# Kernel tuning notes

Measured on AMD Instinct MI355X. Metric: run time of the kernel, lower is better.

Reference implementation:

```python
import jax, jax.numpy as jnp
import numpy as np

B, H, NQ, NK, DH, DD = 2, 16, 1024, 1024, 128, 8


def setup_inputs() -> dict:
    key = jax.random.key(0)
    ks = jax.random.split(key, 10)
    f = lambda kk, s: jax.random.normal(kk, s, dtype=jnp.float32)
    return {
        "q": f(ks[0], (B, H, NQ, DH)),
        "k": f(ks[1], (B, H, NK, DH)),
        "v": f(ks[2], (B, H, NK, DH)),
        "c": jnp.ones((1,), jnp.float32),  # leaky constant; unused (is_leaky=False)
        "d_q": f(ks[3], (B, NQ, DD)),
        "d_k_top": f(ks[4], (B, NK, DD)),
        "d_k_bot": f(ks[5], (B, NK, DD)),
        "d_k_score": jax.random.uniform(ks[6], (B, NK, 2, 1), dtype=jnp.float32),
        "w_w": f(ks[7], (DD, H)) * 0.1,
        "b_w": jnp.zeros((H,), jnp.float32),
        "w_b": f(ks[8], (DD, H)) * 0.1,
        "b_b": jnp.zeros((H,), jnp.float32),
    }


def reference(q, k, v, c, d_q, d_k_top, d_k_bot, d_k_score, w_w, b_w, w_b, b_b):
    # scaled dot-product scores: [B,H,Nq,Nk]
    scale = 1.0 / jnp.sqrt(jnp.asarray(q.shape[-1], q.dtype))
    scores = jnp.einsum('bhqd,bhkd->bhqk', q, k) * scale

    # pairwise relative maps: [B,Nq,Nk,2,Dd]
    dm = jnp.stack(
        [d_q[:, :, None, :] - d_k_top[:, None, :, :],
         d_q[:, :, None, :] - d_k_bot[:, None, :, :]], axis=3)
    # interpolate top/bot with sampler scores d_k_score [B,Nk,2,1] -> [B,Nq,Nk,Dd]
    dm = (dm * d_k_score[:, None]).sum(axis=3)

    # tiny per-head projections Dd -> H, then gate (softplus) and bias
    dw = jax.nn.softplus(dm @ w_w + b_w)        # [B,Nq,Nk,H]
    db = dm @ w_b + b_b                          # [B,Nq,Nk,H]
    scores = scores * dw.transpose(0, 3, 1, 2) + db.transpose(0, 3, 1, 2)

    p = jax.nn.softmax(scores, axis=-1)          # probability_function (non-leaky)
    out = p @ v                                  # [B,H,Nq,dh]
    return out, p
```

## Files before the change

kernel.cpp:

```cpp
#include <hip/hip_runtime.h>

typedef short short8 __attribute__((ext_vector_type(8)));
typedef float f32x4 __attribute__((ext_vector_type(4)));

constexpr int Bc = 2, Hc = 16, NQc = 1024, NKc = 1024, DHc = 128;
constexpr int BQ = 16;
constexpr int PBP = 1032;
constexpr size_t KBF_ELEMS = (size_t)Bc * Hc * NKc * DHc;

__device__ __forceinline__ unsigned cvtpk(float a, float b) {
  unsigned r;
  asm("v_cvt_pk_bf16_f32 %0, %1, %2" : "=v"(r) : "v"(a), "v"(b));
  return r;
}
__device__ __forceinline__ unsigned long long pack4(float a, float b, float c, float d) {
  return (unsigned long long)cvtpk(a, b) | ((unsigned long long)cvtpk(c, d) << 32);
}
__device__ __forceinline__ float bfbits(unsigned u) {
  union { unsigned x; float f; } w; w.x = u; return w.f;
}

typedef __attribute__((address_space(1))) const unsigned int glb_u32;
typedef __attribute__((address_space(3))) unsigned int lds_u32;
__device__ __forceinline__ void gl16(const void* g, void* l) {
  __builtin_amdgcn_global_load_lds((glb_u32*)g, (lds_u32*)l, 16, 0, 0);
}

__global__ __launch_bounds__(256) void prep(const float* __restrict__ km,
                                            const float* __restrict__ vm,
                                            unsigned short* __restrict__ kbf,
                                            unsigned short* __restrict__ vtb) {
  const int blk = blockIdx.x, t = threadIdx.x;
  if (blk < 1024) {
    __shared__ float tile[64][65];
    const int bh = blk >> 5, tl = blk & 31;
    const int k0 = (tl & 15) * 64, d0 = (tl >> 4) * 64;
    const float* vsrc = vm + ((size_t)bh * NKc + k0) * DHc + d0;
    {
      int j = t & 63, i0 = t >> 6;
#pragma unroll
      for (int s = 0; s < 16; ++s) {
        int i = i0 + s * 4;
        tile[i][j] = vsrc[(size_t)i * DHc + j];
      }
    }
    __syncthreads();
    unsigned short* vdst = vtb + ((size_t)bh * DHc + d0) * NKc + k0;
    {
      int i2 = (t & 15) * 4, j0 = t >> 4;
#pragma unroll
      for (int s = 0; s < 4; ++s) {
        int j2 = j0 + s * 16;
        float a0 = tile[i2 + 0][j2], a1 = tile[i2 + 1][j2];
        float a2 = tile[i2 + 2][j2], a3 = tile[i2 + 3][j2];
        *(unsigned long long*)(vdst + (size_t)j2 * NKc + i2) = pack4(a0, a1, a2, a3);
      }
    }
  } else {
    const float4* kf4 = (const float4*)km;
#pragma unroll
    for (int rep = 0; rep < 2; ++rep) {
      size_t g = (size_t)(blk - 1024) * 256 + t + (size_t)rep * 524288;
      float4 f = kf4[g];
      *(unsigned long long*)(kbf + g * 4) = pack4(f.x, f.y, f.z, f.w);
    }
  }
}

__global__ __launch_bounds__(512, 4) void attn_main(
    const float* __restrict__ qm, const unsigned short* __restrict__ kbf,
    const unsigned short* __restrict__ vtb,
    const float* __restrict__ dq, const float* __restrict__ dkt, const float* __restrict__ dkb,
    const float* __restrict__ dks, const float* __restrict__ ww, const float* __restrict__ bw,
    const float* __restrict__ wb, const float* __restrict__ bb,
    float* __restrict__ outp, float* __restrict__ pp)
{
  __shared__ __align__(16) unsigned short kv[16384];
  __shared__ __align__(16) unsigned short pbs[BQ * PBP];
  __shared__ float e0s[1024], cws[1024], cbs[1024];
  __shared__ float aws[BQ], abs_[BQ];
  __shared__ float redm[128], redl[128];

  const int wg = blockIdx.x;
  const int bid = (wg & 7) * 256 + (wg >> 3);
  const int qt = bid & 63, h = (bid >> 6) & 15, b = bid >> 10;
  const int q0 = qt * BQ;
  const int t = threadIdx.x, wv = t >> 6, lane = t & 63;
  const int hi = lane >> 4, lo = lane & 15;
  const int rb = hi << 2;
  const int bh = b * Hc + h;

  {
    float whc[8], wbc[8];
#pragma unroll
    for (int d = 0; d < 8; ++d) { whc[d] = ww[d * Hc + h]; wbc[d] = wb[d * Hc + h]; }
    float bwh = bw[h], bbh = bb[h];
#pragma unroll
    for (int rep = 0; rep < 2; ++rep) {
      int kk = t + rep * 512;
      const float* sc = dks + ((size_t)b * NKc + kk) * 2;
      float s0 = sc[0], s1 = sc[1];
      const float* tp = dkt + ((size_t)b * NKc + kk) * 8;
      const float* bp = dkb + ((size_t)b * NKc + kk) * 8;
      float4 t0 = *(const float4*)tp, t1 = *(const float4*)(tp + 4);
      float4 b0 = *(const float4*)bp, b1 = *(const float4*)(bp + 4);
      float tv[8] = {t0.x, t0.y, t0.z, t0.w, t1.x, t1.y, t1.z, t1.w};
      float bv[8] = {b0.x, b0.y, b0.z, b0.w, b1.x, b1.y, b1.z, b1.w};
      float cw = 0.f, cb = 0.f;
#pragma unroll
      for (int d = 0; d < 8; ++d) {
        float dk = tv[d] * s0 + bv[d] * s1;
        cw += dk * whc[d];
        cb += dk * wbc[d];
      }
      e0s[kk] = s0 + s1;
      cws[kk] = cw - bwh;
      cbs[kk] = cb - bbh;
    }
    if (t < BQ) {
      const float* dqr = dq + ((size_t)b * NQc + q0 + t) * 8;
      float4 a = *(const float4*)dqr, b4 = *(const float4*)(dqr + 4);
      float dv[8] = {a.x, a.y, a.z, a.w, b4.x, b4.y, b4.z, b4.w};
      float saw = 0.f, sab = 0.f;
#pragma unroll
      for (int d = 0; d < 8; ++d) { saw += dv[d] * whc[d]; sab += dv[d] * wbc[d]; }
      aws[t] = saw; abs_[t] = sab;
    }
  }

  short8 qf[4];
  {
    const float* qg = qm + ((size_t)bh * NQc + q0 + lo) * DHc + hi * 8;
#pragma unroll
    for (int kk = 0; kk < 4; ++kk) {
      float4 a = *(const float4*)(qg + kk * 32);
      float4 c = *(const float4*)(qg + kk * 32 + 4);
      union { short8 v; unsigned long long u[2]; } q8;
      q8.u[0] = pack4(a.x, a.y, a.z, a.w);
      q8.u[1] = pack4(c.x, c.y, c.z, c.w);
      qf[kk] = q8.v;
    }
  }

  const float scale = 0.08838834764831845f;
  const unsigned short* kg = kbf + (size_t)bh * NKc * DHc;
  const unsigned short* vtg = vtb + (size_t)bh * DHc * NKc;

  const unsigned short* ksrc[4];
  const unsigned short* vsrc[4];
  char* ldst[4];
#pragma unroll
  for (int r = 0; r < 4; ++r) {
    int base = ((r << 3) + wv) << 10;
    int F = base + (lane << 4);
    int kr = F >> 8;
    int gslot = ((F >> 4) & 15) ^ (kr & 15);
    ksrc[r] = kg + ((size_t)kr << 7) + (gslot << 3);
    vsrc[r] = vtg + ((size_t)kr << 10) + (gslot << 3);
    ldst[r] = (char*)kv + base;
  }
  const int kr16 = (wv << 4) + lo;
  int qoff[4];
#pragma unroll
  for (int kk = 0; kk < 4; ++kk)
    qoff[kk] = (kr16 << 7) + (((((kk << 2) + hi)) ^ (kr16 & 15)) << 3);

  __syncthreads();
  float aw4[4], ab4[4];
#pragma unroll
  for (int i = 0; i < 4; ++i) { aw4[i] = aws[rb + i]; ab4[i] = abs_[rb + i]; }

  f32x4 sacc[8];
#pragma unroll 1
  for (int kc = 0; kc < 8; ++kc) {
    __syncthreads();
#pragma unroll
    for (int r = 0; r < 4; ++r)
      gl16(ksrc[r] + ((size_t)kc << 14), ldst[r]);
    __syncthreads();
    f32x4 acc = {0.f, 0.f, 0.f, 0.f};
#pragma unroll
    for (int kk = 0; kk < 4; ++kk)
      acc = __builtin_amdgcn_mfma_f32_16x16x32_bf16(qf[kk], *(const short8*)&kv[qoff[kk]], acc, 0, 0, 0);
    int cg = (kc << 7) + kr16;
    float e0 = e0s[cg], cw2 = cws[cg], cb2 = cbs[cg];
#pragma unroll
    for (int i = 0; i < 4; ++i) {
      float s = acc[i] * scale;
      float x = fmaf(e0, aw4[i], -cw2);
      float ex = __expf(x);
      float sp = (x > 20.f) ? x : __logf(1.f + ex);
      acc[i] = fmaf(s, sp, fmaf(e0, ab4[i], -cb2));
    }
    sacc[kc] = acc;
  }

  float m4[4], inv4[4];
#pragma unroll
  for (int i = 0; i < 4; ++i) {
    float pm = sacc[0][i];
#pragma unroll
    for (int kc = 1; kc < 8; ++kc) pm = fmaxf(pm, sacc[kc][i]);
    pm = fmaxf(pm, __shfl_xor(pm, 1, 64));
    pm = fmaxf(pm, __shfl_xor(pm, 2, 64));
    pm = fmaxf(pm, __shfl_xor(pm, 4, 64));
    pm = fmaxf(pm, __shfl_xor(pm, 8, 64));
    m4[i] = pm;
  }
  if (lo == 0) {
#pragma unroll
    for (int i = 0; i < 4; ++i) redm[(wv << 4) + rb + i] = m4[i];
  }
  __syncthreads();
#pragma unroll
  for (int i = 0; i < 4; ++i) {
    float m = redm[rb + i];
#pragma unroll
    for (int w = 1; w < 8; ++w) m = fmaxf(m, redm[(w << 4) + rb + i]);
    m4[i] = m;
  }
#pragma unroll
  for (int i = 0; i < 4; ++i) {
    float pl = 0.f;
#pragma unroll
    for (int kc = 0; kc < 8; ++kc) {
      float e = __expf(sacc[kc][i] - m4[i]);
      sacc[kc][i] = e;
      pl += e;
    }
    pl += __shfl_xor(pl, 1, 64);
    pl += __shfl_xor(pl, 2, 64);
    pl += __shfl_xor(pl, 4, 64);
    pl += __shfl_xor(pl, 8, 64);
    inv4[i] = pl;
  }
  if (lo == 0) {
#pragma unroll
    for (int i = 0; i < 4; ++i) redl[(wv << 4) + rb + i] = inv4[i];
  }
  __syncthreads();
#pragma unroll
  for (int i = 0; i < 4; ++i) {
    float l = redl[rb + i];
#pragma unroll
    for (int w = 1; w < 8; ++w) l += redl[(w << 4) + rb + i];
    inv4[i] = 1.f / l;
  }
#pragma unroll
  for (int i = 0; i < 4; ++i) {
    int prow = (rb + i) * PBP + kr16;
    float iv = inv4[i];
#pragma unroll
    for (int k2 = 0; k2 < 4; ++k2) {
      unsigned u = cvtpk(sacc[2 * k2][i] * iv, sacc[2 * k2 + 1][i] * iv);
      pbs[prow + ((2 * k2) << 7)] = (unsigned short)u;
      pbs[prow + ((2 * k2 + 1) << 7)] = (unsigned short)(u >> 16);
    }
  }

  const int pA = lo * PBP + (hi << 3);
  const int prow_w = t >> 5, pc4 = (t & 31) * 4;
  const unsigned short* pbr = &pbs[prow_w * PBP + pc4];
  float* pgl = pp + ((size_t)bh * NQc + q0 + prow_w) * (size_t)NKc + pc4;
  f32x4 oacc = {0.f, 0.f, 0.f, 0.f};
#pragma unroll 1
  for (int vc = 0; vc < 8; ++vc) {
    __syncthreads();
#pragma unroll
    for (int r = 0; r < 4; ++r)
      gl16(vsrc[r] + (vc << 7), ldst[r]);
    {
      unsigned long long u = *(const unsigned long long*)(pbr + (vc << 7));
      unsigned l32 = (unsigned)u, h32 = (unsigned)(u >> 32);
      float4 o;
      o.x = bfbits(l32 << 16);
      o.y = bfbits(l32 & 0xffff0000u);
      o.z = bfbits(h32 << 16);
      o.w = bfbits(h32 & 0xffff0000u);
      *(float4*)(pgl + (vc << 7)) = o;
    }
    __syncthreads();
#pragma unroll
    for (int kt = 0; kt < 4; ++kt) {
      short8 af = *(const short8*)&pbs[pA + (vc << 7) + (kt << 5)];
      short8 bf = *(const short8*)&kv[qoff[kt]];
      oacc = __builtin_amdgcn_mfma_f32_16x16x32_bf16(af, bf, oacc, 0, 0, 0);
    }
  }

#pragma unroll
  for (int i = 0; i < 4; ++i)
    outp[((size_t)bh * NQc + q0 + rb + i) * DHc + kr16] = oacc[i];
}

extern "C" void kernel_launch(void* const* d_in, const int* in_sizes, int n_in,
                              void* d_out, int out_size, void* d_ws, size_t ws_size,
                              hipStream_t stream) {
  (void)in_sizes; (void)n_in; (void)out_size; (void)ws_size;
  const float* q   = (const float*)d_in[0];
  const float* k   = (const float*)d_in[1];
  const float* v   = (const float*)d_in[2];
  const float* dq  = (const float*)d_in[4];
  const float* dkt = (const float*)d_in[5];
  const float* dkb = (const float*)d_in[6];
  const float* dks = (const float*)d_in[7];
  const float* ww  = (const float*)d_in[8];
  const float* bw  = (const float*)d_in[9];
  const float* wb  = (const float*)d_in[10];
  const float* bb  = (const float*)d_in[11];
  float* outp = (float*)d_out;
  float* pp   = outp + (size_t)Bc * Hc * NQc * DHc;

  unsigned short* kbf = (unsigned short*)d_ws;
  unsigned short* vtb = kbf + KBF_ELEMS;

  hipLaunchKernelGGL(prep, dim3(3072), dim3(256), 0, stream, k, v, kbf, vtb);
  hipLaunchKernelGGL(attn_main, dim3(2048), dim3(512), 0, stream,
                     q, kbf, vtb, dq, dkt, dkb, dks, ww, bw, wb, bb, outp, pp);
}
```

Before: 278.3 us.

## Double-buffer K/V LDS tiles with manual vmcnt waits and raw barriers

Splits the K/V LDS staging area into two buffers and issues global-to-LDS loads two chunks ahead, so memory transfers overlap with MFMA and softplus work. The next V chunks are prefetched during the final score iterations. Full __syncthreads calls are replaced with explicit s_waitcnt vmcnt/lgkmcnt plus s_barrier so waits can be partial. The extra 32KB of LDS lowers the occupancy hint from 4 to 2 blocks per CU, and the hand-counted vmcnt values interact with the p global stores, which makes correctness fragile.

```diff
diff --git a/kernel.cpp b/kernel.cpp
--- a/kernel.cpp
+++ b/kernel.cpp
@@ -7,6 +7,11 @@
 constexpr int BQ = 16;
 constexpr int PBP = 1032;
 constexpr size_t KBF_ELEMS = (size_t)Bc * Hc * NKc * DHc;
+
+#define BARRIER() __builtin_amdgcn_s_barrier()
+#define WAITV(n) asm volatile("s_waitcnt vmcnt(" #n ")" ::: "memory")
+#define WAITL0() asm volatile("s_waitcnt lgkmcnt(0)" ::: "memory")
+#define SCHED0() __builtin_amdgcn_sched_barrier(0)
 
 __device__ __forceinline__ unsigned cvtpk(float a, float b) {
   unsigned r;
@@ -67,7 +72,7 @@
   }
 }
 
-__global__ __launch_bounds__(512, 4) void attn_main(
+__global__ __launch_bounds__(512, 2) void attn_main(
     const float* __restrict__ qm, const unsigned short* __restrict__ kbf,
     const unsigned short* __restrict__ vtb,
     const float* __restrict__ dq, const float* __restrict__ dkt, const float* __restrict__ dkb,
@@ -75,7 +80,7 @@
     const float* __restrict__ wb, const float* __restrict__ bb,
     float* __restrict__ outp, float* __restrict__ pp)
 {
-  __shared__ __align__(16) unsigned short kv[16384];
+  __shared__ __align__(16) unsigned short kv[2][16384];
   __shared__ __align__(16) unsigned short pbs[BQ * PBP];
   __shared__ float e0s[1024], cws[1024], cbs[1024];
   __shared__ float aws[BQ], abs_[BQ];
@@ -148,7 +153,7 @@
 
   const unsigned short* ksrc[4];
   const unsigned short* vsrc[4];
-  char* ldst[4];
+  int boff[4];
 #pragma unroll
   for (int r = 0; r < 4; ++r) {
     int base = ((r << 3) + wv) << 10;
@@ -157,7 +162,7 @@
     int gslot = ((F >> 4) & 15) ^ (kr & 15);
     ksrc[r] = kg + ((size_t)kr << 7) + (gslot << 3);
     vsrc[r] = vtg + ((size_t)kr << 10) + (gslot << 3);
-    ldst[r] = (char*)kv + base;
+    boff[r] = base;
   }
   const int kr16 = (wv << 4) + lo;
   int qoff[4];
@@ -169,19 +174,22 @@
   float aw4[4], ab4[4];
 #pragma unroll
   for (int i = 0; i < 4; ++i) { aw4[i] = aws[rb + i]; ab4[i] = abs_[rb + i]; }
+
+#pragma unroll
+  for (int r = 0; r < 4; ++r) gl16(ksrc[r], (char*)&kv[0][0] + boff[r]);
+#pragma unroll
+  for (int r = 0; r < 4; ++r) gl16(ksrc[r] + (1 << 14), (char*)&kv[1][0] + boff[r]);
 
   f32x4 sacc[8];
 #pragma unroll 1
   for (int kc = 0; kc < 8; ++kc) {
-    __syncthreads();
-#pragma unroll
-    for (int r = 0; r < 4; ++r)
-      gl16(ksrc[r] + ((size_t)kc << 14), ldst[r]);
-    __syncthreads();
+    const int cur = kc & 1;
+    WAITV(4); SCHED0();
+    BARRIER();
     f32x4 acc = {0.f, 0.f, 0.f, 0.f};
 #pragma unroll
     for (int kk = 0; kk < 4; ++kk)
-      acc = __builtin_amdgcn_mfma_f32_16x16x32_bf16(qf[kk], *(const short8*)&kv[qoff[kk]], acc, 0, 0, 0);
+      acc = __builtin_amdgcn_mfma_f32_16x16x32_bf16(qf[kk], *(const short8*)&kv[cur][qoff[kk]], acc, 0, 0, 0);
     int cg = (kc << 7) + kr16;
     float e0 = e0s[cg], cw2 = cws[cg], cb2 = cbs[cg];
 #pragma unroll
@@ -193,6 +201,16 @@
       acc[i] = fmaf(s, sp, fmaf(e0, ab4[i], -cb2));
     }
     sacc[kc] = acc;
+    WAITL0(); SCHED0();
+    BARRIER();
+    if (kc < 6) {
+#pragma unroll
+      for (int r = 0; r < 4; ++r) gl16(ksrc[r] + ((size_t)(kc + 2) << 14), (char*)&kv[cur][0] + boff[r]);
+    } else {
+      int vc0 = kc - 6;
+#pragma unroll
+      for (int r = 0; r < 4; ++r) gl16(vsrc[r] + (vc0 << 7), (char*)&kv[cur][0] + boff[r]);
+    }
   }
 
   float m4[4], inv4[4];
@@ -211,7 +229,7 @@
 #pragma unroll
     for (int i = 0; i < 4; ++i) redm[(wv << 4) + rb + i] = m4[i];
   }
-  __syncthreads();
+  WAITL0(); SCHED0(); BARRIER();
 #pragma unroll
   for (int i = 0; i < 4; ++i) {
     float m = redm[rb + i];
@@ -238,7 +256,7 @@
 #pragma unroll
     for (int i = 0; i < 4; ++i) redl[(wv << 4) + rb + i] = inv4[i];
   }
-  __syncthreads();
+  WAITL0(); SCHED0(); BARRIER();
 #pragma unroll
   for (int i = 0; i < 4; ++i) {
     float l = redl[rb + i];
@@ -257,6 +275,7 @@
       pbs[prow + ((2 * k2 + 1) << 7)] = (unsigned short)(u >> 16);
     }
   }
+  WAITL0();
 
   const int pA = lo * PBP + (hi << 3);
   const int prow_w = t >> 5, pc4 = (t & 31) * 4;
@@ -264,27 +283,35 @@
   float* pgl = pp + ((size_t)bh * NQc + q0 + prow_w) * (size_t)NKc + pc4;
   f32x4 oacc = {0.f, 0.f, 0.f, 0.f};
 #pragma unroll 1
-  for (int vc = 0; vc < 8; ++vc) {
-    __syncthreads();
-#pragma unroll
-    for (int r = 0; r < 4; ++r)
-      gl16(vsrc[r] + (vc << 7), ldst[r]);
+  for (int vc = 8; vc < 16; ++vc) {
+    const int cur = vc & 1;
+    const int vc0 = vc - 8;
+    if (vc == 8)      { WAITV(4); }
+    else if (vc == 15){ WAITV(1); }
+    else              { WAITV(5); }
+    SCHED0();
+    BARRIER();
+#pragma unroll
+    for (int kt = 0; kt < 4; ++kt) {
+      short8 af = *(const short8*)&pbs[pA + (vc0 << 7) + (kt << 5)];
+      short8 bf = *(const short8*)&kv[cur][qoff[kt]];
+      oacc = __builtin_amdgcn_mfma_f32_16x16x32_bf16(af, bf, oacc, 0, 0, 0);
+    }
     {
-      unsigned long long u = *(const unsigned long long*)(pbr + (vc << 7));
+      unsigned long long u = *(const unsigned long long*)(pbr + (vc0 << 7));
       unsigned l32 = (unsigned)u, h32 = (unsigned)(u >> 32);
       float4 o;
       o.x = bfbits(l32 << 16);
       o.y = bfbits(l32 & 0xffff0000u);
       o.z = bfbits(h32 << 16);
       o.w = bfbits(h32 & 0xffff0000u);
-      *(float4*)(pgl + (vc << 7)) = o;
-    }
-    __syncthreads();
-#pragma unroll
-    for (int kt = 0; kt < 4; ++kt) {
-      short8 af = *(const short8*)&pbs[pA + (vc << 7) + (kt << 5)];
-      short8 bf = *(const short8*)&kv[qoff[kt]];
-      oacc = __builtin_amdgcn_mfma_f32_16x16x32_bf16(af, bf, oacc, 0, 0, 0);
+      *(float4*)(pgl + (vc0 << 7)) = o;
+    }
+    WAITL0(); SCHED0();
+    BARRIER();
+    if (vc0 + 2 < 8) {
+#pragma unroll
+      for (int r = 0; r < 4; ++r) gl16(vsrc[r] + ((vc0 + 2) << 7), (char*)&kv[cur][0] + boff[r]);
     }
   }
 
```

Result: slower. 319.2 us (+14.7%).

## Pre-swizzle K/V into MFMA fragment order and load directly to registers

Applied to the files above, without the earlier changes.

The prep kernel now writes bf16 K and V in the exact per-lane MFMA fragment order, so attn_main loads operands straight from global memory into registers with double-buffered prefetch instead of staging them through LDS with global_load_lds. The large P buffer in LDS is replaced by a small double-buffered per-chunk tile, and the P store to global is software-pipelined one chunk behind. Barriers become raw s_barrier calls with explicit lgkmcnt waits. This removes LDS staging and most block-wide syncs and shrinks LDS use, which may raise occupancy, but it increases register pressure and relies on uncoalesced-looking fragment loads being cached well.

```diff
diff --git a/kernel.cpp b/kernel.cpp
--- a/kernel.cpp
+++ b/kernel.cpp
@@ -5,8 +5,12 @@
 
 constexpr int Bc = 2, Hc = 16, NQc = 1024, NKc = 1024, DHc = 128;
 constexpr int BQ = 16;
-constexpr int PBP = 1032;
-constexpr size_t KBF_ELEMS = (size_t)Bc * Hc * NKc * DHc;
+constexpr int PBP = 136;
+constexpr size_t FRAG_ELEMS = (size_t)Bc * Hc * NKc * DHc;
+
+#define BARRIER() __builtin_amdgcn_s_barrier()
+#define WAITL0() asm volatile("s_waitcnt lgkmcnt(0)" ::: "memory")
+#define SCHED0() __builtin_amdgcn_sched_barrier(0)
 
 __device__ __forceinline__ unsigned cvtpk(float a, float b) {
   unsigned r;
@@ -20,16 +24,10 @@
   union { unsigned x; float f; } w; w.x = u; return w.f;
 }
 
-typedef __attribute__((address_space(1))) const unsigned int glb_u32;
-typedef __attribute__((address_space(3))) unsigned int lds_u32;
-__device__ __forceinline__ void gl16(const void* g, void* l) {
-  __builtin_amdgcn_global_load_lds((glb_u32*)g, (lds_u32*)l, 16, 0, 0);
-}
-
 __global__ __launch_bounds__(256) void prep(const float* __restrict__ km,
                                             const float* __restrict__ vm,
-                                            unsigned short* __restrict__ kbf,
-                                            unsigned short* __restrict__ vtb) {
+                                            unsigned short* __restrict__ kf2,
+                                            unsigned short* __restrict__ vf2) {
   const int blk = blockIdx.x, t = threadIdx.x;
   if (blk < 1024) {
     __shared__ float tile[64][65];
@@ -45,38 +43,48 @@
       }
     }
     __syncthreads();
-    unsigned short* vdst = vtb + ((size_t)bh * DHc + d0) * NKc + k0;
-    {
-      int i2 = (t & 15) * 4, j0 = t >> 4;
-#pragma unroll
-      for (int s = 0; s < 4; ++s) {
-        int j2 = j0 + s * 16;
-        float a0 = tile[i2 + 0][j2], a1 = tile[i2 + 1][j2];
-        float a2 = tile[i2 + 2][j2], a3 = tile[i2 + 3][j2];
-        *(unsigned long long*)(vdst + (size_t)j2 * NKc + i2) = pack4(a0, a1, a2, a3);
-      }
+    const int vc = k0 >> 7, ktb = (k0 >> 5) & 3, wvb = d0 >> 4;
+    unsigned short* vdst = vf2 + ((size_t)bh << 17);
+#pragma unroll
+    for (int s2 = 0; s2 < 2; ++s2) {
+      int ts = s2 * 256 + t;
+      int wvl = ts >> 7, ktl = (ts >> 6) & 1, hii = (ts >> 4) & 3, loo = ts & 15;
+      int seg = ((vc * 4 + ktb + ktl) * 8 + wvb + wvl) * 64 + (hii << 4) + loo;
+      int kl = ktl * 32 + hii * 8;
+      int dl = wvl * 16 + loo;
+      float a0 = tile[kl + 0][dl], a1 = tile[kl + 1][dl], a2 = tile[kl + 2][dl], a3 = tile[kl + 3][dl];
+      float a4 = tile[kl + 4][dl], a5 = tile[kl + 5][dl], a6 = tile[kl + 6][dl], a7 = tile[kl + 7][dl];
+      unsigned long long u0 = pack4(a0, a1, a2, a3), u1 = pack4(a4, a5, a6, a7);
+      *(unsigned long long*)(vdst + (size_t)seg * 8) = u0;
+      *(unsigned long long*)(vdst + (size_t)seg * 8 + 4) = u1;
     }
   } else {
-    const float4* kf4 = (const float4*)km;
-#pragma unroll
-    for (int rep = 0; rep < 2; ++rep) {
-      size_t g = (size_t)(blk - 1024) * 256 + t + (size_t)rep * 524288;
-      float4 f = kf4[g];
-      *(unsigned long long*)(kbf + g * 4) = pack4(f.x, f.y, f.z, f.w);
+    const int blk2 = blk - 1024;
+    const int bh = blk2 >> 3, kc = blk2 & 7;
+    const float* ks = km + ((size_t)bh * NKc + kc * 128) * DHc;
+    unsigned short* kdst = kf2 + ((size_t)(bh * 8 + kc)) * 16384;
+#pragma unroll
+    for (int s8 = 0; s8 < 8; ++s8) {
+      int s = s8 * 256 + t;
+      int kk = s >> 9, wvv = (s >> 6) & 7, hii = (s >> 4) & 3, loo = s & 15;
+      const float* sp = ks + (size_t)(wvv * 16 + loo) * DHc + kk * 32 + hii * 8;
+      float4 A = *(const float4*)sp, B4 = *(const float4*)(sp + 4);
+      unsigned long long u0 = pack4(A.x, A.y, A.z, A.w), u1 = pack4(B4.x, B4.y, B4.z, B4.w);
+      *(unsigned long long*)(kdst + (size_t)s * 8) = u0;
+      *(unsigned long long*)(kdst + (size_t)s * 8 + 4) = u1;
     }
   }
 }
 
 __global__ __launch_bounds__(512, 4) void attn_main(
-    const float* __restrict__ qm, const unsigned short* __restrict__ kbf,
-    const unsigned short* __restrict__ vtb,
+    const float* __restrict__ qm, const unsigned short* __restrict__ kf2,
+    const unsigned short* __restrict__ vf2,
     const float* __restrict__ dq, const float* __restrict__ dkt, const float* __restrict__ dkb,
     const float* __restrict__ dks, const float* __restrict__ ww, const float* __restrict__ bw,
     const float* __restrict__ wb, const float* __restrict__ bb,
     float* __restrict__ outp, float* __restrict__ pp)
 {
-  __shared__ __align__(16) unsigned short kv[16384];
-  __shared__ __align__(16) unsigned short pbs[BQ * PBP];
+  __shared__ __align__(16) unsigned short pb[2][BQ * PBP];
   __shared__ float e0s[1024], cws[1024], cbs[1024];
   __shared__ float aws[BQ], abs_[BQ];
   __shared__ float redm[128], redl[128];
@@ -89,6 +97,29 @@
   const int hi = lane >> 4, lo = lane & 15;
   const int rb = hi << 2;
   const int bh = b * Hc + h;
+  const int kr16 = (wv << 4) + lo;
+
+  const unsigned short* kfb = kf2 + ((size_t)bh << 17) + (((wv << 6) + lane) << 3);
+  const unsigned short* vfb = vf2 + ((size_t)bh << 17) + (((wv << 6) + lane) << 3);
+
+  short8 kf[2][4];
+#pragma unroll
+  for (int kk = 0; kk < 4; ++kk)
+    kf[0][kk] = *(const short8*)(kfb + (kk << 12));
+
+  short8 qf[4];
+  {
+    const float* qg = qm + ((size_t)bh * NQc + q0 + lo) * DHc + hi * 8;
+#pragma unroll
+    for (int kk = 0; kk < 4; ++kk) {
+      float4 a = *(const float4*)(qg + kk * 32);
+      float4 c = *(const float4*)(qg + kk * 32 + 4);
+      union { short8 v; unsigned long long u[2]; } q8;
+      q8.u[0] = pack4(a.x, a.y, a.z, a.w);
+      q8.u[1] = pack4(c.x, c.y, c.z, c.w);
+      qf[kk] = q8.v;
+    }
+  }
 
   {
     float whc[8], wbc[8];
@@ -127,61 +158,26 @@
       aws[t] = saw; abs_[t] = sab;
     }
   }
-
-  short8 qf[4];
-  {
-    const float* qg = qm + ((size_t)bh * NQc + q0 + lo) * DHc + hi * 8;
-#pragma unroll
-    for (int kk = 0; kk < 4; ++kk) {
-      float4 a = *(const float4*)(qg + kk * 32);
-      float4 c = *(const float4*)(qg + kk * 32 + 4);
-      union { short8 v; unsigned long long u[2]; } q8;
-      q8.u[0] = pack4(a.x, a.y, a.z, a.w);
-      q8.u[1] = pack4(c.x, c.y, c.z, c.w);
-      qf[kk] = q8.v;
-    }
-  }
+  WAITL0(); SCHED0(); BARRIER();
+
+  float aw4[4], ab4[4];
+#pragma unroll
+  for (int i = 0; i < 4; ++i) { aw4[i] = aws[rb + i]; ab4[i] = abs_[rb + i]; }
 
   const float scale = 0.08838834764831845f;
-  const unsigned short* kg = kbf + (size_t)bh * NKc * DHc;
-  const unsigned short* vtg = vtb + (size_t)bh * DHc * NKc;
-
-  const unsigned short* ksrc[4];
-  const unsigned short* vsrc[4];
-  char* ldst[4];
-#pragma unroll
-  for (int r = 0; r < 4; ++r) {
-    int base = ((r << 3) + wv) << 10;
-    int F = base + (lane << 4);
-    int kr = F >> 8;
-    int gslot = ((F >> 4) & 15) ^ (kr & 15);
-    ksrc[r] = kg + ((size_t)kr << 7) + (gslot << 3);
-    vsrc[r] = vtg + ((size_t)kr << 10) + (gslot << 3);
-    ldst[r] = (char*)kv + base;
-  }
-  const int kr16 = (wv << 4) + lo;
-  int qoff[4];
-#pragma unroll
-  for (int kk = 0; kk < 4; ++kk)
-    qoff[kk] = (kr16 << 7) + (((((kk << 2) + hi)) ^ (kr16 & 15)) << 3);
-
-  __syncthreads();
-  float aw4[4], ab4[4];
-#pragma unroll
-  for (int i = 0; i < 4; ++i) { aw4[i] = aws[rb + i]; ab4[i] = abs_[rb + i]; }
 
   f32x4 sacc[8];
-#pragma unroll 1
+#pragma unroll
   for (int kc = 0; kc < 8; ++kc) {
-    __syncthreads();
-#pragma unroll
-    for (int r = 0; r < 4; ++r)
-      gl16(ksrc[r] + ((size_t)kc << 14), ldst[r]);
-    __syncthreads();
+    if (kc < 7) {
+#pragma unroll
+      for (int kk = 0; kk < 4; ++kk)
+        kf[(kc & 1) ^ 1][kk] = *(const short8*)(kfb + ((((kc + 1) << 2) + kk) << 12));
+    }
     f32x4 acc = {0.f, 0.f, 0.f, 0.f};
 #pragma unroll
     for (int kk = 0; kk < 4; ++kk)
-      acc = __builtin_amdgcn_mfma_f32_16x16x32_bf16(qf[kk], *(const short8*)&kv[qoff[kk]], acc, 0, 0, 0);
+      acc = __builtin_amdgcn_mfma_f32_16x16x32_bf16(qf[kk], kf[kc & 1][kk], acc, 0, 0, 0);
     int cg = (kc << 7) + kr16;
     float e0 = e0s[cg], cw2 = cws[cg], cb2 = cbs[cg];
 #pragma unroll
@@ -195,6 +191,11 @@
     sacc[kc] = acc;
   }
 
+  short8 vf[2][4];
+#pragma unroll
+  for (int kt = 0; kt < 4; ++kt)
+    vf[0][kt] = *(const short8*)(vfb + (kt << 12));
+
   float m4[4], inv4[4];
 #pragma unroll
   for (int i = 0; i < 4; ++i) {
@@ -211,7 +212,7 @@
 #pragma unroll
     for (int i = 0; i < 4; ++i) redm[(wv << 4) + rb + i] = m4[i];
   }
-  __syncthreads();
+  WAITL0(); SCHED0(); BARRIER();
 #pragma unroll
   for (int i = 0; i < 4; ++i) {
     float m = redm[rb + i];
@@ -238,7 +239,7 @@
 #pragma unroll
     for (int i = 0; i < 4; ++i) redl[(wv << 4) + rb + i] = inv4[i];
   }
-  __syncthreads();
+  WAITL0(); SCHED0(); BARRIER();
 #pragma unroll
   for (int i = 0; i < 4; ++i) {
     float l = redl[rb + i];
@@ -246,46 +247,51 @@
     for (int w = 1; w < 8; ++w) l += redl[(w << 4) + rb + i];
     inv4[i] = 1.f / l;
   }
-#pragma unroll
-  for (int i = 0; i < 4; ++i) {
-    int prow = (rb + i) * PBP + kr16;
-    float iv = inv4[i];
-#pragma unroll
-    for (int k2 = 0; k2 < 4; ++k2) {
-      unsigned u = cvtpk(sacc[2 * k2][i] * iv, sacc[2 * k2 + 1][i] * iv);
-      pbs[prow + ((2 * k2) << 7)] = (unsigned short)u;
-      pbs[prow + ((2 * k2 + 1) << 7)] = (unsigned short)(u >> 16);
-    }
-  }
-
-  const int pA = lo * PBP + (hi << 3);
+
   const int prow_w = t >> 5, pc4 = (t & 31) * 4;
-  const unsigned short* pbr = &pbs[prow_w * PBP + pc4];
   float* pgl = pp + ((size_t)bh * NQc + q0 + prow_w) * (size_t)NKc + pc4;
   f32x4 oacc = {0.f, 0.f, 0.f, 0.f};
-#pragma unroll 1
+#pragma unroll
   for (int vc = 0; vc < 8; ++vc) {
-    __syncthreads();
-#pragma unroll
-    for (int r = 0; r < 4; ++r)
-      gl16(vsrc[r] + (vc << 7), ldst[r]);
-    {
-      unsigned long long u = *(const unsigned long long*)(pbr + (vc << 7));
+    if (vc < 7) {
+#pragma unroll
+      for (int kt = 0; kt < 4; ++kt)
+        vf[(vc & 1) ^ 1][kt] = *(const short8*)(vfb + ((((vc + 1) << 2) + kt) << 12));
+    }
+    if (vc > 0) {
+      unsigned long long u = *(const unsigned long long*)&pb[(vc + 1) & 1][prow_w * PBP + pc4];
       unsigned l32 = (unsigned)u, h32 = (unsigned)(u >> 32);
       float4 o;
       o.x = bfbits(l32 << 16);
       o.y = bfbits(l32 & 0xffff0000u);
       o.z = bfbits(h32 << 16);
       o.w = bfbits(h32 & 0xffff0000u);
-      *(float4*)(pgl + (vc << 7)) = o;
-    }
-    __syncthreads();
+      *(float4*)(pgl + ((vc - 1) << 7)) = o;
+    }
+    {
+      unsigned u01 = cvtpk(sacc[vc][0] * inv4[0], sacc[vc][1] * inv4[1]);
+      unsigned u23 = cvtpk(sacc[vc][2] * inv4[2], sacc[vc][3] * inv4[3]);
+      pb[vc & 1][(rb + 0) * PBP + kr16] = (unsigned short)u01;
+      pb[vc & 1][(rb + 1) * PBP + kr16] = (unsigned short)(u01 >> 16);
+      pb[vc & 1][(rb + 2) * PBP + kr16] = (unsigned short)u23;
+      pb[vc & 1][(rb + 3) * PBP + kr16] = (unsigned short)(u23 >> 16);
+    }
+    WAITL0(); SCHED0(); BARRIER();
 #pragma unroll
     for (int kt = 0; kt < 4; ++kt) {
-      short8 af = *(const short8*)&pbs[pA + (vc << 7) + (kt << 5)];
-      short8 bf = *(const short8*)&kv[qoff[kt]];
-      oacc = __builtin_amdgcn_mfma_f32_16x16x32_bf16(af, bf, oacc, 0, 0, 0);
-    }
+      short8 af = *(const short8*)&pb[vc & 1][lo * PBP + (kt << 5) + (hi << 3)];
+      oacc = __builtin_amdgcn_mfma_f32_16x16x32_bf16(af, vf[vc & 1][kt], oacc, 0, 0, 0);
+    }
+  }
+  {
+    unsigned long long u = *(const unsigned long long*)&pb[1][prow_w * PBP + pc4];
+    unsigned l32 = (unsigned)u, h32 = (unsigned)(u >> 32);
+    float4 o;
+    o.x = bfbits(l32 << 16);
+    o.y = bfbits(l32 & 0xffff0000u);
+    o.z = bfbits(h32 << 16);
+    o.w = bfbits(h32 & 0xffff0000u);
+    *(float4*)(pgl + (7 << 7)) = o;
   }
 
 #pragma unroll
@@ -311,10 +317,10 @@
   float* outp = (float*)d_out;
   float* pp   = outp + (size_t)Bc * Hc * NQc * DHc;
 
-  unsigned short* kbf = (unsigned short*)d_ws;
-  unsigned short* vtb = kbf + KBF_ELEMS;
-
-  hipLaunchKernelGGL(prep, dim3(3072), dim3(256), 0, stream, k, v, kbf, vtb);
+  unsigned short* kf2 = (unsigned short*)d_ws;
+  unsigned short* vf2 = kf2 + FRAG_ELEMS;
+
+  hipLaunchKernelGGL(prep, dim3(1280), dim3(256), 0, stream, k, v, kf2, vf2);
   hipLaunchKernelGGL(attn_main, dim3(2048), dim3(512), 0, stream,
-                     q, kbf, vtb, dq, dkt, dkb, dks, ww, bw, wb, bb, outp, pp);
-}
+                     q, kf2, vf2, dq, dkt, dkb, dks, ww, bw, wb, bb, outp, pp);
+}
```

Measured after the change: 257.9 us. 1.08x faster.
